# Kernel tuning notes

Hardware: AMD Instinct MI355X
Metric: run time of the kernel (lower is better)

## Reference

```python
import jax, jax.numpy as jnp
import numpy as np

_HIST_BINS = 64
TOP_K_FRAC = 0.125
HIST_THRESHOLD = 2048


def setup_inputs() -> dict:
    key = jax.random.key(0)
    B, S = 256, 131072
    importance = jax.random.normal(key, (B, S), dtype=jnp.float32)
    return {"importance": importance, "S": S}


def reference(importance, S):
    # importance: [B, S] float32; S: python int
    K = max(1, int(TOP_K_FRAC * S))
    if S > HIST_THRESHOLD:
        # Histogram bookkeeping path (computed but unused by the original module;
        # reproduced here for faithfulness to the source's memory traffic).
        imin = jnp.min(importance, axis=-1, keepdims=True)  # [B,1]
        imax = jnp.max(importance, axis=-1, keepdims=True)  # [B,1]
        rng = jnp.clip(imax - imin, 1e-8, None)
        bin_idx = ((importance - imin) / rng * (_HIST_BINS - 1)).astype(jnp.int32)
        bin_idx = jnp.clip(bin_idx, 0, _HIST_BINS - 1)  # [B,S]
        B = importance.shape[0]
        rows = jnp.arange(B)[:, None]  # [B,1] broadcast against [B,S]
        hist = jnp.zeros((B, _HIST_BINS), dtype=jnp.int32).at[rows, bin_idx].add(1)
        del hist  # dead value, exactly as in the torch source
    _, top_idx = jax.lax.top_k(importance, K)  # [B,K] indices into last dim
    return (top_idx, K)
```

## Files before the change

kernel.cpp:

```cpp
#include <hip/hip_runtime.h>
#include <stdint.h>


#define S_LEN   131072
#define K_SEL   16384
#define NBINS   8192
#define LOWBITS 19
#define IDXMASK 0x1FFFFu
#define CAND_CAP 20480
#define SORT_CAP 4096
#define DIRECT_MAX 256
#define HCAP 96
#define PC_LANE 48
#define SEGROW  (1024 * PC_LANE)
#define NITER   (S_LEN / 4 / 1024)
#define U0_THRESH 0xBF880000u
#define BU0 (U0_THRESH >> LOWBITS)

__device__ __forceinline__ unsigned int ordered_u32(float f) {
  unsigned int x = __float_as_uint(f);
  unsigned int mask = (unsigned int)((int)x >> 31) | 0x80000000u;
  return x ^ mask;
}

__device__ __forceinline__ void suffix_scan_8k(const unsigned int* h,
                                               unsigned int* sfx,
                                               unsigned int* waveTot,
                                               unsigned int* sb1p,
                                               int tid, int lane, int wave) {
  if (tid == 0) *sb1p = 0xFFFFFFFFu;
  uint4 c0 = *(const uint4*)&h[tid * 8];
  uint4 c1 = *(const uint4*)&h[tid * 8 + 4];
  unsigned int v[8] = {c0.x, c0.y, c0.z, c0.w, c1.x, c1.y, c1.z, c1.w};
#pragma unroll
  for (int s = 6; s >= 0; --s) v[s] += v[s + 1];
  unsigned int tot = v[0];
  unsigned int suf = tot;
#pragma unroll
  for (int d = 1; d < 64; d <<= 1) {
    unsigned int o = __shfl_down(suf, d, 64);
    if (lane + d < 64) suf += o;
  }
  if (lane == 0) waveTot[wave] = suf;
  __syncthreads();
  unsigned int carry = 0;
  for (int w2 = wave + 1; w2 < 16; ++w2) carry += waveTot[w2];
  unsigned int addv = (suf - tot) + carry;
  {
    uint4 o0 = make_uint4(v[0] + addv, v[1] + addv, v[2] + addv, v[3] + addv);
    uint4 o1 = make_uint4(v[4] + addv, v[5] + addv, v[6] + addv, v[7] + addv);
    *(uint4*)&sfx[tid * 8]     = o0;
    *(uint4*)&sfx[tid * 8 + 4] = o1;
  }
  __syncthreads();
#pragma unroll
  for (int s = 0; s < 8; ++s) {
    int b = tid * 8 + s;
    unsigned int cur = sfx[b];
    unsigned int nxt = (b + 1 < NBINS) ? sfx[b + 1] : 0u;
    if (cur >= K_SEL && nxt < K_SEL) *sb1p = (unsigned int)b;
  }
  __syncthreads();
}

__global__ __launch_bounds__(1024)
void topk_kernel(const float* __restrict__ in,
                 unsigned long long* __restrict__ pairs,
                 unsigned long long* __restrict__ cand,
                 int* __restrict__ out, int B, long long out_size) {
  const int row  = blockIdx.x;
  const int tid  = threadIdx.x;
  const int lane = tid & 63, wave = tid >> 6;
  __shared__ unsigned int  h[NBINS];
  __shared__ unsigned int  sfx[NBINS];
  __shared__ unsigned int  skey2[SORT_CAP];
  __shared__ unsigned char sdig2[SORT_CAP];
  __shared__ unsigned int  ssfx[257];
  __shared__ unsigned int  scur[256];
  __shared__ unsigned int  segTot[4];
  __shared__ unsigned int  waveTot[16];
  __shared__ uint2         lheavy[HCAP];
  __shared__ unsigned int  sb1, sbmax, nH, ovf;

  for (int i = tid; i < NBINS; i += 1024) h[i] = 0;
  if (tid == 0) { nH = 0; ovf = 0; }
  __syncthreads();

  const float4* p = (const float4*)(in + (size_t)row * S_LEN);
  unsigned long long* segT = pairs + (size_t)row * SEGROW + tid;
  unsigned int cnt = 0;

#define PROC1(U, IDX) do {                                                   \
    unsigned int u_ = (U);                                                   \
    if (u_ >= U0_THRESH) {                                                   \
      atomicAdd(&h[u_ >> LOWBITS], 1u);                                      \
      if (cnt < PC_LANE)                                                     \
        segT[(size_t)cnt * 1024] =                                           \
            ((unsigned long long)u_ << 17) |                                 \
            (unsigned long long)(IDXMASK - (unsigned int)(IDX));             \
      ++cnt;                                                                 \
    } } while (0)

#define PROC4(V, I4) do { int idx0_ = (I4) * 4;                              \
    PROC1(ordered_u32((V).x), idx0_ + 0);                                    \
    PROC1(ordered_u32((V).y), idx0_ + 1);                                    \
    PROC1(ordered_u32((V).z), idx0_ + 2);                                    \
    PROC1(ordered_u32((V).w), idx0_ + 3); } while (0)

#pragma unroll 2
  for (int it = 0; it < NITER; it += 4) {
    int i0 = it * 1024 + tid;
    float4 L0 = p[i0];
    float4 L1 = p[i0 + 1024];
    float4 L2 = p[i0 + 2048];
    float4 L3 = p[i0 + 3072];
    PROC4(L0, i0);
    PROC4(L1, i0 + 1024);
    PROC4(L2, i0 + 2048);
    PROC4(L3, i0 + 3072);
  }
  if (cnt > PC_LANE) ovf = 1u;
  __syncthreads();

  suffix_scan_8k(h, sfx, waveTot, &sb1, tid, lane, wave);
  bool fast = (sb1 != 0xFFFFFFFFu);
  if (!fast) {
    for (int it = 0; it < NITER; ++it) {
      float4 v4 = p[it * 1024 + tid];
      float f[4] = {v4.x, v4.y, v4.z, v4.w};
#pragma unroll
      for (int e = 0; e < 4; ++e) {
        unsigned int u = ordered_u32(f[e]);
        if (u < U0_THRESH) atomicAdd(&h[u >> LOWBITS], 1u);
      }
    }
    __syncthreads();
    suffix_scan_8k(h, sfx, waveTot, &sb1, tid, lane, wave);
  }
  const unsigned int b1 = sb1;
  fast = fast && (ovf == 0u);

  {
    unsigned int e8[8], s8[8];
#pragma unroll
    for (int j = 0; j < 8; ++j) {
      int i = tid + j * 1024;
      e8[j] = sfx[i];
      s8[j] = (i + 1 < NBINS) ? sfx[i + 1] : 0u;
    }
#pragma unroll
    for (int j = 0; j < 8; ++j) {
      int i = tid + j * 1024;
      h[i] = s8[j];
      if (e8[j] > 0u && s8[j] == 0u) sbmax = (unsigned int)i;
      if ((unsigned int)i >= b1) {
        unsigned int c2 = e8[j] - s8[j];
        if (c2 > DIRECT_MAX) {
          unsigned int p2 = atomicAdd(&nH, 1u);
          if (p2 < HCAP) lheavy[p2] = make_uint2(s8[j], e8[j]);
        }
      }
    }
  }
  __syncthreads();

  unsigned long long* c = cand + (size_t)row * CAND_CAP;
  if (fast) {
    for (unsigned int i = 0; i < cnt; ++i) {
      unsigned long long k = segT[(size_t)i * 1024];
      unsigned int b = (unsigned int)(k >> 36);
      if (b >= b1) {
        unsigned int pos = atomicAdd(&h[b], 1u);
        if (pos < CAND_CAP) c[pos] = k;
      }
    }
  } else {
    for (int it = 0; it < NITER; ++it) {
      int i4 = it * 1024 + tid;
      float4 v4 = p[i4];
      int idx0 = i4 * 4;
      float f[4] = {v4.x, v4.y, v4.z, v4.w};
#pragma unroll
      for (int e = 0; e < 4; ++e) {
        unsigned int u = ordered_u32(f[e]);
        unsigned int b = u >> LOWBITS;
        if (b >= b1) {
          unsigned int pos = atomicAdd(&h[b], 1u);
          unsigned long long key =
              ((unsigned long long)u << 17) |
              (unsigned long long)(IDXMASK - (unsigned int)(idx0 + e));
          if (pos < CAND_CAP) c[pos] = key;
        }
      }
    }
  }
  if (row == 0 && tid == 0) {
    long long pos = (long long)B * K_SEL;
    if (pos < out_size) out[pos] = K_SEL;
  }
  __syncthreads();

  int* orow = out + (size_t)row * K_SEL;

  const unsigned int nHv = (nH < HCAP) ? nH : HCAP;
  for (unsigned int hi = 0; hi < nHv; ++hi) {
    const uint2 be = lheavy[hi];
    const unsigned int start = be.x;
    unsigned int count = be.y - be.x;
    if (count > SORT_CAP) count = SORT_CAP;
    const unsigned long long* cc = c + start;

    unsigned long long me[4];
#pragma unroll
    for (int j = 0; j < 4; ++j) {
      unsigned int i = (unsigned int)tid + 1024u * j;
      me[j] = (i < count) ? cc[i] : 0ull;
    }
    if (tid < 256) scur[tid] = 0;
    __syncthreads();
#pragma unroll
    for (int j = 0; j < 4; ++j) {
      unsigned int i = (unsigned int)tid + 1024u * j;
      if (i < count) atomicAdd(&scur[(unsigned int)(me[j] >> 28) & 255u], 1u);
    }
    __syncthreads();
    unsigned int sufH = 0;
    if (tid < 256) {
      sufH = scur[tid];
#pragma unroll
      for (int d = 1; d < 64; d <<= 1) {
        unsigned int o = __shfl_down(sufH, d, 64);
        if (lane + d < 64) sufH += o;
      }
      if (lane == 0) segTot[wave] = sufH;
    }
    __syncthreads();
    if (tid < 256) {
      unsigned int carry = 0;
      for (int w2 = wave + 1; w2 < 4; ++w2) carry += segTot[w2];
      ssfx[tid] = sufH + carry;
      if (tid == 0) ssfx[256] = 0;
    }
    __syncthreads();
    if (tid < 256) scur[tid] = ssfx[tid + 1];
    __syncthreads();
#pragma unroll
    for (int j = 0; j < 4; ++j) {
      unsigned int i = (unsigned int)tid + 1024u * j;
      if (i < count) {
        unsigned long long k = me[j];
        unsigned int d = (unsigned int)(k >> 28) & 255u;
        unsigned int p2 = atomicAdd(&scur[d], 1u);
        skey2[p2] = (unsigned int)k & 0x0FFFFFFFu;
        sdig2[p2] = (unsigned char)d;
      }
    }
    __syncthreads();
    for (unsigned int p2 = tid; p2 < count; p2 += 1024) {
      unsigned int k = skey2[p2];
      unsigned int d = sdig2[p2];
      unsigned int lo = ssfx[d + 1], hi2 = ssfx[d];
      unsigned int r = 0;
      for (unsigned int q = lo; q < hi2; ++q) r += (skey2[q] > k) ? 1u : 0u;
      unsigned int pos = start + lo + r;
      if (pos < K_SEL)
        orow[pos] = (int)(IDXMASK - (k & IDXMASK));
    }
    __syncthreads();
  }

  const unsigned int bmaxv = sbmax;
  for (unsigned int b = b1 + (unsigned int)wave; b <= bmaxv; b += 16u) {
    unsigned int end   = sfx[b];
    unsigned int start = (b + 1 < NBINS) ? sfx[b + 1] : 0u;
    unsigned int count = end - start;
    if (count == 0u || count > DIRECT_MAX) continue;
    const unsigned long long* cc = c + start;
    if (count <= 64) {
      unsigned long long me = ((unsigned int)lane < count) ? cc[lane] : 0ull;
      unsigned int r = 0;
      for (int l = 0; l < 64; ++l)
        r += (__shfl(me, l, 64) > me) ? 1u : 0u;
      if ((unsigned int)lane < count) {
        unsigned int pos = start + r;
        if (pos < K_SEL)
          orow[pos] = (int)(IDXMASK - ((unsigned int)me & IDXMASK));
      }
    } else if (count <= 128) {
      unsigned long long me[2];
#pragma unroll
      for (int e = 0; e < 2; ++e) {
        unsigned int i = (unsigned int)lane + 64u * e;
        me[e] = (i < count) ? cc[i] : 0ull;
      }
      unsigned int r[2] = {0u, 0u};
#pragma unroll
      for (int e = 0; e < 2; ++e) {
        for (int l = 0; l < 64; ++l) {
          unsigned long long kj = __shfl(me[e], l, 64);
#pragma unroll
          for (int e2 = 0; e2 < 2; ++e2) r[e2] += (kj > me[e2]) ? 1u : 0u;
        }
      }
#pragma unroll
      for (int e = 0; e < 2; ++e) {
        unsigned int i = (unsigned int)lane + 64u * e;
        if (i < count) {
          unsigned int pos = start + r[e];
          if (pos < K_SEL)
            orow[pos] = (int)(IDXMASK - ((unsigned int)me[e] & IDXMASK));
        }
      }
    } else {
      unsigned long long me[4];
#pragma unroll
      for (int e = 0; e < 4; ++e) {
        unsigned int i = (unsigned int)lane + 64u * e;
        me[e] = (i < count) ? cc[i] : 0ull;
      }
      unsigned int r[4] = {0u, 0u, 0u, 0u};
#pragma unroll
      for (int e = 0; e < 4; ++e) {
        for (int l = 0; l < 64; ++l) {
          unsigned long long kj = __shfl(me[e], l, 64);
#pragma unroll
          for (int e2 = 0; e2 < 4; ++e2) r[e2] += (kj > me[e2]) ? 1u : 0u;
        }
      }
#pragma unroll
      for (int e = 0; e < 4; ++e) {
        unsigned int i = (unsigned int)lane + 64u * e;
        if (i < count) {
          unsigned int pos = start + r[e];
          if (pos < K_SEL)
            orow[pos] = (int)(IDXMASK - ((unsigned int)me[e] & IDXMASK));
        }
      }
    }
  }
#undef PROC1
#undef PROC4
}

extern "C" void kernel_launch(void* const* d_in, const int* in_sizes, int n_in,
                              void* d_out, int out_size, void* d_ws, size_t ws_size,
                              hipStream_t stream) {
  const float* importance = (const float*)d_in[0];
  int B = in_sizes[0] / S_LEN;
  if (B < 1) B = 1;
  (void)n_in; (void)ws_size;

  size_t pairBytes = (size_t)B * SEGROW * sizeof(unsigned long long);
  char* base = (char*)d_ws;
  unsigned long long* pairs = (unsigned long long*)base;
  unsigned long long* cand  = (unsigned long long*)(base + pairBytes);
  int* out = (int*)d_out;

  topk_kernel<<<dim3(B), dim3(1024), 0, stream>>>(
      importance, pairs, cand, out, B, (long long)out_size);
}
```

Baseline: 321.5 us.

## Split top-k into multi-block candidate capture kernel and per-row finish kernel

After: 284.1 us. 1.13x faster.

```diff
diff --git a/kernel.cpp b/kernel.cpp
--- a/kernel.cpp
+++ b/kernel.cpp
@@ -11,16 +11,64 @@
 #define SORT_CAP 4096
 #define DIRECT_MAX 256
 #define HCAP 96
-#define PC_LANE 48
-#define SEGROW  (1024 * PC_LANE)
-#define NITER   (S_LEN / 4 / 1024)
 #define U0_THRESH 0xBF880000u
 #define BU0 (U0_THRESH >> LOWBITS)
+#define NCH1    16
+#define CH1     (S_LEN / NCH1)
+#define K1IT    (CH1 / 4 / 256)
+#define PBUF_CAP 2048
+#define POOL_CAP 24576
 
 __device__ __forceinline__ unsigned int ordered_u32(float f) {
   unsigned int x = __float_as_uint(f);
   unsigned int mask = (unsigned int)((int)x >> 31) | 0x80000000u;
   return x ^ mask;
+}
+
+__global__ __launch_bounds__(256, 4)
+void capture_kernel(const float* __restrict__ in,
+                    unsigned long long* __restrict__ pool,
+                    unsigned int* __restrict__ rowcur,
+                    unsigned int* __restrict__ rowflag, int B) {
+  const int row   = blockIdx.x % B;
+  const int chunk = blockIdx.x / B;
+  const int tid   = threadIdx.x;
+  __shared__ unsigned long long pbuf[PBUF_CAP];
+  __shared__ unsigned int scnt, sgbase;
+  if (tid == 0) scnt = 0;
+  __syncthreads();
+
+  const float4* p = (const float4*)(in + (size_t)row * S_LEN + (size_t)chunk * CH1);
+  float4 L[K1IT];
+#pragma unroll
+  for (int it = 0; it < K1IT; ++it) L[it] = p[it * 256 + tid];
+#pragma unroll
+  for (int it = 0; it < K1IT; ++it) {
+    const int idx0 = chunk * CH1 + (it * 256 + tid) * 4;
+    const float f[4] = {L[it].x, L[it].y, L[it].z, L[it].w};
+#pragma unroll
+    for (int e = 0; e < 4; ++e) {
+      unsigned int u = ordered_u32(f[e]);
+      if (u >= U0_THRESH) {
+        unsigned int pos = atomicAdd(&scnt, 1u);
+        if (pos < PBUF_CAP)
+          pbuf[pos] = ((unsigned long long)u << 17) |
+                      (unsigned long long)(IDXMASK - (unsigned int)(idx0 + e));
+      }
+    }
+  }
+  __syncthreads();
+  unsigned int cnt = scnt, over = 0;
+  if (cnt > PBUF_CAP) { cnt = PBUF_CAP; over = 1; }
+  if (tid == 0) sgbase = atomicAdd(&rowcur[row], cnt);
+  __syncthreads();
+  const unsigned int gbase = sgbase;
+  unsigned int wc = cnt;
+  if (gbase >= POOL_CAP) wc = 0;
+  else if (gbase + cnt > POOL_CAP) wc = POOL_CAP - gbase;
+  if (tid == 0 && (over || wc < cnt)) rowflag[row] = 1u;
+  unsigned long long* dst = pool + (size_t)row * POOL_CAP + gbase;
+  for (unsigned int i = tid; i < wc; i += 256) dst[i] = pbuf[i];
 }
 
 __device__ __forceinline__ void suffix_scan_8k(const unsigned int* h,
@@ -64,10 +112,12 @@
 }
 
 __global__ __launch_bounds__(1024)
-void topk_kernel(const float* __restrict__ in,
-                 unsigned long long* __restrict__ pairs,
-                 unsigned long long* __restrict__ cand,
-                 int* __restrict__ out, int B, long long out_size) {
+void finish_kernel(const float* __restrict__ in,
+                   const unsigned long long* __restrict__ pool,
+                   const unsigned int* __restrict__ rowcur,
+                   const unsigned int* __restrict__ rowflag,
+                   unsigned long long* __restrict__ cand,
+                   int* __restrict__ out, int B, long long out_size) {
   const int row  = blockIdx.x;
   const int tid  = threadIdx.x;
   const int lane = tid & 63, wave = tid >> 6;
@@ -80,55 +130,38 @@
   __shared__ unsigned int  segTot[4];
   __shared__ unsigned int  waveTot[16];
   __shared__ uint2         lheavy[HCAP];
-  __shared__ unsigned int  sb1, sbmax, nH, ovf;
+  __shared__ unsigned int  sb1, sbmax, nH;
 
   for (int i = tid; i < NBINS; i += 1024) h[i] = 0;
-  if (tid == 0) { nH = 0; ovf = 0; }
-  __syncthreads();
-
+  if (tid == 0) nH = 0;
+  __syncthreads();
+
+  unsigned int n = rowcur[row];
+  const bool flagged = (rowflag[row] != 0u) || (n > POOL_CAP);
   const float4* p = (const float4*)(in + (size_t)row * S_LEN);
-  unsigned long long* segT = pairs + (size_t)row * SEGROW + tid;
-  unsigned int cnt = 0;
-
-#define PROC1(U, IDX) do {                                                   \
-    unsigned int u_ = (U);                                                   \
-    if (u_ >= U0_THRESH) {                                                   \
-      atomicAdd(&h[u_ >> LOWBITS], 1u);                                      \
-      if (cnt < PC_LANE)                                                     \
-        segT[(size_t)cnt * 1024] =                                           \
-            ((unsigned long long)u_ << 17) |                                 \
-            (unsigned long long)(IDXMASK - (unsigned int)(IDX));             \
-      ++cnt;                                                                 \
-    } } while (0)
-
-#define PROC4(V, I4) do { int idx0_ = (I4) * 4;                              \
-    PROC1(ordered_u32((V).x), idx0_ + 0);                                    \
-    PROC1(ordered_u32((V).y), idx0_ + 1);                                    \
-    PROC1(ordered_u32((V).z), idx0_ + 2);                                    \
-    PROC1(ordered_u32((V).w), idx0_ + 3); } while (0)
-
-#pragma unroll 2
-  for (int it = 0; it < NITER; it += 4) {
-    int i0 = it * 1024 + tid;
-    float4 L0 = p[i0];
-    float4 L1 = p[i0 + 1024];
-    float4 L2 = p[i0 + 2048];
-    float4 L3 = p[i0 + 3072];
-    PROC4(L0, i0);
-    PROC4(L1, i0 + 1024);
-    PROC4(L2, i0 + 2048);
-    PROC4(L3, i0 + 3072);
-  }
-  if (cnt > PC_LANE) ovf = 1u;
-  __syncthreads();
-
-  suffix_scan_8k(h, sfx, waveTot, &sb1, tid, lane, wave);
-  bool fast = (sb1 != 0xFFFFFFFFu);
-  if (!fast) {
-    for (int it = 0; it < NITER; ++it) {
+  const unsigned long long* pl = pool + (size_t)row * POOL_CAP;
+
+  if (!flagged) {
+    for (unsigned int i = tid; i < n; i += 1024)
+      atomicAdd(&h[(unsigned int)(pl[i] >> 36)], 1u);
+  } else {
+    for (int it = 0; it < 32; ++it) {
       float4 v4 = p[it * 1024 + tid];
       float f[4] = {v4.x, v4.y, v4.z, v4.w};
 #pragma unroll
+      for (int e = 0; e < 4; ++e)
+        atomicAdd(&h[ordered_u32(f[e]) >> LOWBITS], 1u);
+    }
+  }
+  __syncthreads();
+
+  suffix_scan_8k(h, sfx, waveTot, &sb1, tid, lane, wave);
+  bool found1 = (sb1 != 0xFFFFFFFFu);
+  if (!found1) {
+    for (int it = 0; it < 32; ++it) {
+      float4 v4 = p[it * 1024 + tid];
+      float f[4] = {v4.x, v4.y, v4.z, v4.w};
+#pragma unroll
       for (int e = 0; e < 4; ++e) {
         unsigned int u = ordered_u32(f[e]);
         if (u < U0_THRESH) atomicAdd(&h[u >> LOWBITS], 1u);
@@ -138,27 +171,18 @@
     suffix_scan_8k(h, sfx, waveTot, &sb1, tid, lane, wave);
   }
   const unsigned int b1 = sb1;
-  fast = fast && (ovf == 0u);
-
-  {
-    unsigned int e8[8], s8[8];
-#pragma unroll
-    for (int j = 0; j < 8; ++j) {
-      int i = tid + j * 1024;
-      e8[j] = sfx[i];
-      s8[j] = (i + 1 < NBINS) ? sfx[i + 1] : 0u;
-    }
-#pragma unroll
-    for (int j = 0; j < 8; ++j) {
-      int i = tid + j * 1024;
-      h[i] = s8[j];
-      if (e8[j] > 0u && s8[j] == 0u) sbmax = (unsigned int)i;
-      if ((unsigned int)i >= b1) {
-        unsigned int c2 = e8[j] - s8[j];
-        if (c2 > DIRECT_MAX) {
-          unsigned int p2 = atomicAdd(&nH, 1u);
-          if (p2 < HCAP) lheavy[p2] = make_uint2(s8[j], e8[j]);
-        }
+  const bool fast = found1 && !flagged;
+
+  for (int i = tid; i < NBINS; i += 1024) {
+    unsigned int end   = sfx[i];
+    unsigned int start = (i + 1 < NBINS) ? sfx[i + 1] : 0u;
+    h[i] = start;
+    if (end > 0u && start == 0u) sbmax = (unsigned int)i;
+    if ((unsigned int)i >= b1) {
+      unsigned int c2 = end - start;
+      if (c2 > DIRECT_MAX) {
+        unsigned int p2 = atomicAdd(&nH, 1u);
+        if (p2 < HCAP) lheavy[p2] = make_uint2(start, end);
       }
     }
   }
@@ -166,8 +190,8 @@
 
   unsigned long long* c = cand + (size_t)row * CAND_CAP;
   if (fast) {
-    for (unsigned int i = 0; i < cnt; ++i) {
-      unsigned long long k = segT[(size_t)i * 1024];
+    for (unsigned int i = tid; i < n; i += 1024) {
+      unsigned long long k = pl[i];
       unsigned int b = (unsigned int)(k >> 36);
       if (b >= b1) {
         unsigned int pos = atomicAdd(&h[b], 1u);
@@ -175,7 +199,7 @@
       }
     }
   } else {
-    for (int it = 0; it < NITER; ++it) {
+    for (int it = 0; it < 32; ++it) {
       int i4 = it * 1024 + tid;
       float4 v4 = p[i4];
       int idx0 = i4 * 4;
@@ -338,8 +362,6 @@
       }
     }
   }
-#undef PROC1
-#undef PROC4
 }
 
 extern "C" void kernel_launch(void* const* d_in, const int* in_sizes, int n_in,
@@ -350,12 +372,18 @@
   if (B < 1) B = 1;
   (void)n_in; (void)ws_size;
 
-  size_t pairBytes = (size_t)B * SEGROW * sizeof(unsigned long long);
+  size_t poolBytes = (size_t)B * POOL_CAP * sizeof(unsigned long long);
+  size_t candBytes = (size_t)B * CAND_CAP * sizeof(unsigned long long);
   char* base = (char*)d_ws;
-  unsigned long long* pairs = (unsigned long long*)base;
-  unsigned long long* cand  = (unsigned long long*)(base + pairBytes);
+  unsigned long long* pool = (unsigned long long*)base;
+  unsigned long long* cand = (unsigned long long*)(base + poolBytes);
+  unsigned int* rowcur     = (unsigned int*)(base + poolBytes + candBytes);
+  unsigned int* rowflag    = rowcur + B;
   int* out = (int*)d_out;
 
-  topk_kernel<<<dim3(B), dim3(1024), 0, stream>>>(
-      importance, pairs, cand, out, B, (long long)out_size);
-}
+  hipMemsetAsync(rowcur, 0, 2 * (size_t)B * sizeof(unsigned int), stream);
+  capture_kernel<<<dim3(B * NCH1), dim3(256), 0, stream>>>(
+      importance, pool, rowcur, rowflag, B);
+  finish_kernel<<<dim3(B), dim3(1024), 0, stream>>>(
+      importance, pool, rowcur, rowflag, cand, out, B, (long long)out_size);
+}
```
